# Optimization experiments

Measured on AMD Instinct MI355X. Metric: run time of the kernel, lower is better.

## Reference

```python
import jax, jax.numpy as jnp
import numpy as np

B, T, D, H, L = 8, 150, 30, 5, 3
HD = D // H  # 6
ORIG = (300, 74, 35)


def setup_inputs() -> dict:
    key = jax.random.key(0)
    ks = iter(jax.random.split(key, 40))
    def g(shape, s=0.05):
        return jax.random.normal(next(ks), shape, dtype=jnp.float32) * s
    return {
        "x_l": g((B, T, ORIG[0]), 1.0),
        "x_a": g((B, T, ORIG[1]), 1.0),
        "x_v": g((B, T, ORIG[2]), 1.0),
        "Wl": g((D, ORIG[0])),
        "Wa": g((D, ORIG[1])),
        "Wv": g((D, ORIG[2])),
        "in_w": g((2, L, 3 * D, D)),
        "in_b": jnp.zeros((2, L, 3 * D), jnp.float32),
        "out_w": g((2, L, D, D)),
        "out_b": jnp.zeros((2, L, D), jnp.float32),
        "lin1_w": g((2, L, 4 * D, D)),
        "lin1_b": jnp.zeros((2, L, 4 * D), jnp.float32),
        "lin2_w": g((2, L, D, 4 * D)),
        "lin2_b": jnp.zeros((2, L, D), jnp.float32),
        "n1_g": jnp.ones((2, L, D), jnp.float32),
        "n1_b": jnp.zeros((2, L, D), jnp.float32),
        "n2_g": jnp.ones((2, L, D), jnp.float32),
        "n2_b": jnp.zeros((2, L, D), jnp.float32),
        "p1_w": g((2 * D, 2 * D)),
        "p1_b": jnp.zeros((2 * D,), jnp.float32),
        "p2_w": g((2 * D, 2 * D)),
        "p2_b": jnp.zeros((2 * D,), jnp.float32),
        "ow": g((1, 2 * D)),
        "ob": jnp.zeros((1,), jnp.float32),
    }


def _ln(x, g, b, eps=1e-5):
    m = x.mean(-1, keepdims=True)
    v = jnp.var(x, axis=-1, keepdims=True)  # biased var, matches torch LayerNorm
    return (x - m) * jax.lax.rsqrt(v + eps) * g + b


def _heads(x):  # [Tt, B, D] -> [B*H, Tt, HD]
    Tt = x.shape[0]
    return x.reshape(Tt, B * H, HD).transpose(1, 0, 2)


def _layer(x, xk, xv, p):
    iw, ib, ow, ob, w1, b1, w2, b2, g1, bb1, g2, bb2 = p
    res = x
    xn, kn, vn = _ln(x, g1, bb1), _ln(xk, g1, bb1), _ln(xv, g1, bb1)
    q = (xn @ iw[:D].T + ib[:D]) * (HD ** -0.5)
    k = kn @ iw[D:2 * D].T + ib[D:2 * D]
    v = vn @ iw[2 * D:].T + ib[2 * D:]
    qh, kh, vh = _heads(q), _heads(k), _heads(v)
    # trilinear scores: [B*H, Tq, Tk, Tv]
    aw = jnp.einsum('iat,ibt,ict->iabc', qh, kh, vh)
    fused = aw.mean(-1) + aw.max(-1)          # fuse over value axis -> [B*H, Tq, Tk]
    fused = jax.nn.softmax(fused, axis=-1)
    attn = jnp.einsum('iab,ibt->iat', fused, qh)  # NB: original bmm uses q, not v
    attn = attn.transpose(1, 0, 2).reshape(-1, B, D)
    x = res + (attn @ ow.T + ob)
    res = x
    xn = _ln(x, g2, bb2)
    x = jax.nn.relu(xn @ w1.T + b1) @ w2.T + b2
    return res + x


def reference(x_l, x_a, x_v, Wl, Wa, Wv, in_w, in_b, out_w, out_b,
              lin1_w, lin1_b, lin2_w, lin2_b, n1_g, n1_b, n2_g, n2_b,
              p1_w, p1_b, p2_w, p2_b, ow, ob):
    pl = (x_l @ Wl.T).transpose(1, 0, 2)  # [T, B, D] (conv1d k=1, no bias)
    pa = (x_a @ Wa.T).transpose(1, 0, 2)
    pv = (x_v @ Wv.T).transpose(1, 0, 2)
    hs = []
    for s, (kk, vv) in enumerate(((pa, pv), (pv, pa))):
        h = pl
        for l in range(L):
            p = (in_w[s, l], in_b[s, l], out_w[s, l], out_b[s, l],
                 lin1_w[s, l], lin1_b[s, l], lin2_w[s, l], lin2_b[s, l],
                 n1_g[s, l], n1_b[s, l], n2_g[s, l], n2_b[s, l])
            h = _layer(h, kk, vv, p)
        hs.append(h[-1])  # last timestep [B, D]
    last_hs = jnp.concatenate(hs, axis=1)  # [B, 2D]
    proj = jax.nn.relu(last_hs @ p1_w.T + p1_b) @ p2_w.T + p2_b + last_hs
    out = proj @ ow.T + ob
    return (out, last_hs)
```

## Files before the change

### kernel.cpp

```cpp
#include <hip/hip_runtime.h>
#include <math.h>

#define BB 8
#define TT 150
#define DD 30
#define HH 5
#define HD 6
#define LL 3
#define NI 40
#define ROWF (TT*BB*DD)
#define RSTR 8
#define NR 152

typedef _Float16 half8 __attribute__((ext_vector_type(8)));
typedef float f32x16 __attribute__((ext_vector_type(16)));

__device__ __forceinline__ float wsum(float v) {
    #pragma unroll
    for (int m = 32; m > 0; m >>= 1) v += __shfl_xor(v, m, 64);
    return v;
}

__global__ __launch_bounds__(256) void proj3_kernel(
    const float* __restrict__ x_l, const float* __restrict__ x_a, const float* __restrict__ x_v,
    const float* __restrict__ Wl, const float* __restrict__ Wa, const float* __restrict__ Wv,
    float* __restrict__ pl, float* __restrict__ pa, float* __restrict__ pv) {
    int blk = blockIdx.x;
    int which = blk / 300;
    int w = threadIdx.x >> 6, lane = threadIdx.x & 63;
    int rowu = (blk % 300) * 4 + w;
    int t = rowu / BB, b = rowu % BB;
    const float* x = which == 0 ? x_l : (which == 1 ? x_a : x_v);
    const float* W = which == 0 ? Wl : (which == 1 ? Wa : Wv);
    float* out = which == 0 ? pl : (which == 1 ? pa : pv);
    int Cin = which == 0 ? 300 : (which == 1 ? 74 : 35);
    int cst = Cin | 1;
    __shared__ float WS[30 * 301];
    __shared__ float xr[4][304];
    for (int j = threadIdx.x; j < DD * Cin; j += 256)
        WS[(j / Cin) * cst + (j % Cin)] = W[j];
    const float* xp = x + ((size_t)b * TT + t) * Cin;
    for (int j = lane; j < Cin; j += 64) xr[w][j] = xp[j];
    __syncthreads();
    int d = lane >> 1, jh = lane & 1;
    int h1 = Cin >> 1;
    int j0 = jh ? h1 : 0, j1 = jh ? Cin : h1;
    const float* wr = WS + (size_t)(d < DD ? d : 0) * cst;
    float acc = 0.f;
    for (int j = j0; j < j1; j++) acc += xr[w][j] * wr[j];
    acc += __shfl_xor(acc, 1, 64);
    if (jh == 0 && d < DD) out[t * (BB * DD) + b * DD + d] = acc;
}

__global__ __launch_bounds__(256) void kvq0_kernel(
    const float* __restrict__ pl, const float* __restrict__ pa, const float* __restrict__ pv,
    const float* __restrict__ in_w, const float* __restrict__ in_b,
    const float* __restrict__ n1g, const float* __restrict__ n1b,
    float* __restrict__ k_all, float* __restrict__ v_all, float* __restrict__ q) {
    int blk = blockIdx.x;
    int w = threadIdx.x >> 6, lane = threadIdx.x & 63;
    __shared__ float iwS[1800];
    __shared__ float xn[4][2][30];
    if (blk < 1800) {
        int po = blk / 300;
        int s = po / LL;
        int tb = (blk % 300) * 4 + w;
        int t = tb / BB, b = tb % BB;
        const float* xk = (s == 0) ? pa : pv;
        const float* xv = (s == 0) ? pv : pa;
        const float* iw = in_w + (size_t)po * 2700 + 900;
        const float* ib = in_b + (size_t)po * 90;
        const float* g  = n1g + (size_t)po * 30;
        const float* bb = n1b + (size_t)po * 30;
        for (int j = threadIdx.x; j < 1800; j += 256) iwS[j] = iw[j];
        const float* rows[2] = { xk + (size_t)tb * 30, xv + (size_t)tb * 30 };
        for (int r = 0; r < 2; r++) {
            float xval = (lane < 30) ? rows[r][lane] : 0.f;
            float mean = wsum(xval) * (1.f / 30.f);
            float dv = (lane < 30) ? (xval - mean) : 0.f;
            float var = wsum(dv * dv) * (1.f / 30.f);
            float inv = rsqrtf(var + 1e-5f);
            if (lane < 30) xn[w][r][lane] = dv * inv * g[lane] + bb[lane];
        }
        __syncthreads();
        if (lane < 60) {
            int which = lane / 30, dd = lane % 30;
            const float* wr = iwS + lane * 30;
            const float* xv2 = xn[w][which];
            float acc = 0.f;
            #pragma unroll 6
            for (int j = 0; j < 30; j++) acc += wr[j] * xv2[j];
            acc += ib[30 + lane];
            int i = b * HH + dd / HD, hd = dd % HD;
            float* dst = which ? v_all : k_all;
            dst[((size_t)po * NI + i) * (TT * HD) + t * HD + hd] = acc;
        }
    } else {
        int r2 = blk - 1800;
        int s = r2 / 300;
        int tb = (r2 % 300) * 4 + w;
        int t = tb / BB, b = tb % BB;
        int po = s * LL;
        const float* iw = in_w + (size_t)po * 2700;
        const float* ib = in_b + (size_t)po * 90;
        const float* g  = n1g + (size_t)po * 30;
        const float* bb = n1b + (size_t)po * 30;
        for (int j = threadIdx.x; j < 900; j += 256) iwS[j] = iw[j];
        const float* row = pl + (size_t)tb * 30;
        float xval = (lane < 30) ? row[lane] : 0.f;
        float mean = wsum(xval) * (1.f / 30.f);
        float dv = (lane < 30) ? (xval - mean) : 0.f;
        float var = wsum(dv * dv) * (1.f / 30.f);
        float inv = rsqrtf(var + 1e-5f);
        if (lane < 30) xn[w][0][lane] = dv * inv * g[lane] + bb[lane];
        __syncthreads();
        if (lane < 30) {
            const float* wr = iwS + lane * 30;
            float acc = 0.f;
            #pragma unroll 6
            for (int j = 0; j < 30; j++) acc += wr[j] * xn[w][0][j];
            acc = (acc + ib[lane]) * 0.40824829046386307f;
            int i = b * HH + lane / HD, hd = lane % HD;
            q[((size_t)s * NI + i) * (TT * HD) + t * HD + hd] = acc;
        }
    }
}

__global__ __launch_bounds__(256) void score_kernel(
    const float* __restrict__ q, const float* __restrict__ k_all,
    const float* __restrict__ v_all, int l, float* __restrict__ attn) {
    int blk = blockIdx.x;
    int s = blk / 760;
    int rem = blk % 760;
    int i = rem / 19;
    int g = rem % 19;
    int tid = threadIdx.x;
    int wv = tid >> 6, lane = tid & 63;
    int lo = lane & 31, hf = lane >> 5;
    int po = s * LL + l;

    __shared__ __align__(16) _Float16 qsh[NR * RSTR];
    __shared__ __align__(16) _Float16 ksh[NR * RSTR];
    __shared__ __align__(16) _Float16 vsh[NR * RSTR];

    const float* qg = q + (size_t)(s * NI + i) * (TT * HD);
    const float* kg = k_all + (size_t)(po * NI + i) * (TT * HD);
    const float* vg = v_all + (size_t)(po * NI + i) * (TT * HD);
    half8 z8;
    #pragma unroll
    for (int t = 0; t < 8; t++) z8[t] = (_Float16)0.f;
    for (int r = tid; r < NR; r += 256) {
        half8 qa = z8, ka = z8, va = z8;
        if (r < TT) {
            #pragma unroll
            for (int t = 0; t < 6; t++) {
                qa[t] = (_Float16)qg[r * 6 + t];
                ka[t] = (_Float16)kg[r * 6 + t];
                va[t] = (_Float16)vg[r * 6 + t];
            }
        }
        *(half8*)&qsh[r * RSTR] = qa;
        *(half8*)&ksh[r * RSTR] = ka;
        *(half8*)&vsh[r * RSTR] = va;
    }
    __syncthreads();
    if (wv == 0) {
        float v6[6] = {0.f, 0.f, 0.f, 0.f, 0.f, 0.f};
        for (int c = lane; c < TT; c += 64) {
            #pragma unroll
            for (int t = 0; t < 6; t++) v6[t] += (float)vsh[c * RSTR + t];
        }
        #pragma unroll
        for (int m = 32; m > 0; m >>= 1) {
            #pragma unroll
            for (int t = 0; t < 6; t++) v6[t] += __shfl_xor(v6[t], m, 64);
        }
        if (lane < 6) vsh[TT * RSTR + lane] = (_Float16)(v6[lane] * (1.f / TT));
    }
    __syncthreads();

    f32x16 zacc;
    #pragma unroll
    for (int j = 0; j < 16; j++) zacc[j] = 0.f;

    half8 bfrag[5], vhalf[5];
    #pragma unroll
    for (int nt = 0; nt < 5; nt++) {
        int rr = nt * 32 + lo;
        int rc = rr < 151 ? rr : 151;
        half8 kf = *(const half8*)&ksh[rc * RSTR];
        half8 vf = *(const half8*)&vsh[rc * RSTR];
        bfrag[nt] = hf ? z8 : kf;
        vhalf[nt] = hf ? z8 : vf;
    }

    for (int ap = 0; ap < 2; ap++) {
        int a = g * 8 + wv * 2 + ap;
        if (a >= TT) break;
        half8 qav = *(const half8*)&qsh[a * RSTR];
        half8 afrag[5];
        #pragma unroll
        for (int nt = 0; nt < 5; nt++) afrag[nt] = vhalf[nt] * qav;

        float fsc[5];
        #pragma unroll
        for (int nb = 0; nb < 5; nb++) {
            float rm = -INFINITY;
            #pragma unroll
            for (int ma = 0; ma < 4; ma++) {
                f32x16 acc = __builtin_amdgcn_mfma_f32_32x32x16_f16(afrag[ma], bfrag[nb], zacc, 0, 0, 0);
                float m = fmaxf(acc[0], acc[1]);
                #pragma unroll
                for (int j = 2; j < 16; j += 2) m = fmaxf(fmaxf(m, acc[j]), acc[j + 1]);
                rm = fmaxf(rm, m);
            }
            f32x16 a4 = __builtin_amdgcn_mfma_f32_32x32x16_f16(afrag[4], bfrag[nb], zacc, 0, 0, 0);
            float m4 = fmaxf(a4[0], a4[1]);
            #pragma unroll
            for (int j = 2; j < 10; j += 2) m4 = fmaxf(fmaxf(m4, a4[j]), a4[j + 1]);
            float ext = (hf == 0) ? fmaxf(a4[10], a4[11]) : -INFINITY;
            rm = fmaxf(rm, fmaxf(m4, ext));
            float om = __shfl_xor(a4[10], 32, 64);
            float mn = hf ? a4[10] : om;
            rm = fmaxf(rm, __shfl_xor(rm, 32, 64));
            int bcol = nb * 32 + lo;
            fsc[nb] = (bcol < TT) ? (mn + rm) : -INFINITY;
        }
        float m = fsc[0];
        #pragma unroll
        for (int nb = 1; nb < 5; nb++) m = fmaxf(m, fsc[nb]);
        #pragma unroll
        for (int msk = 16; msk > 0; msk >>= 1) m = fmaxf(m, __shfl_xor(m, msk, 64));
        float e[5], es = 0.f;
        #pragma unroll
        for (int nb = 0; nb < 5; nb++) { e[nb] = __expf(fsc[nb] - m); es += e[nb]; }
        #pragma unroll
        for (int msk = 16; msk > 0; msk >>= 1) es += __shfl_xor(es, msk, 64);
        float acc6[6] = {0.f, 0.f, 0.f, 0.f, 0.f, 0.f};
        #pragma unroll
        for (int nb = 0; nb < 5; nb++) {
            int bcol = nb * 32 + lo;
            int bi = (bcol < TT) ? bcol : 0;
            float wgt = e[nb];
            half8 qrow = *(const half8*)&qsh[bi * RSTR];
            #pragma unroll
            for (int t = 0; t < 6; t++) acc6[t] += wgt * (float)qrow[t];
        }
        #pragma unroll
        for (int msk = 16; msk > 0; msk >>= 1) {
            #pragma unroll
            for (int t = 0; t < 6; t++) acc6[t] += __shfl_xor(acc6[t], msk, 64);
        }
        if (lane == 0) {
            float inv = 1.f / es;
            int bo = i / HH, ho = i % HH;
            float* dst = attn + (size_t)s * ROWF + a * (BB * DD) + bo * DD + ho * HD;
            #pragma unroll
            for (int t = 0; t < 6; t++) dst[t] = acc6[t] * inv;
        }
    }
}

__global__ __launch_bounds__(256) void ffnlnq_kernel(
    const float* __restrict__ attn, const float* __restrict__ pl,
    const float* __restrict__ out_w, const float* __restrict__ out_b,
    const float* __restrict__ l1w, const float* __restrict__ l1b,
    const float* __restrict__ l2w, const float* __restrict__ l2b,
    const float* __restrict__ n2g, const float* __restrict__ n2b,
    const float* __restrict__ in_w, const float* __restrict__ in_b,
    const float* __restrict__ n1g, const float* __restrict__ n1b,
    int l, int has_next,
    float* __restrict__ h, float* __restrict__ q) {
    int blk = blockIdx.x;
    int s = blk / 300;
    int w = threadIdx.x >> 6, lane = threadIdx.x & 63;
    int tb = (blk % 300) * 4 + w;
    int t = tb / BB, b = tb % BB;
    int po = s * LL + l;
    const float* ow = out_w + (size_t)po * 900;
    const float* ob = out_b + (size_t)po * 30;
    const float* w1 = l1w + (size_t)po * 3600;
    const float* b1 = l1b + (size_t)po * 120;
    const float* w2 = l2w + (size_t)po * 3600;
    const float* b2 = l2b + (size_t)po * 30;
    const float* g2 = n2g + (size_t)po * 30;
    const float* bb2 = n2b + (size_t)po * 30;
    __shared__ float owS[900];
    __shared__ float w1T[30 * 128];
    __shared__ float w2S[30 * 121];
    __shared__ float iwqS[900];
    __shared__ float arS[4][30], xnS[4][32], hidS[4][120], xqS[4][30];
    for (int j = threadIdx.x; j < 900; j += 256) owS[j] = ow[j];
    for (int j = threadIdx.x; j < 3600; j += 256) w1T[(j % 30) * 128 + (j / 30)] = w1[j];
    for (int j = threadIdx.x; j < 3600; j += 256) w2S[(j / 120) * 121 + (j % 120)] = w2[j];
    if (has_next) {
        const float* iwq = in_w + (size_t)(po + 1) * 2700;
        for (int j = threadIdx.x; j < 900; j += 256) iwqS[j] = iwq[j];
    }
    __syncthreads();
    float* hrow = h + (size_t)s * ROWF + (size_t)tb * 30;
    const float* res = (l == 0) ? (pl + (size_t)tb * 30) : hrow;
    const float* arow = attn + (size_t)s * ROWF + (size_t)tb * 30;
    if (lane < 30) arS[w][lane] = arow[lane];
    float x1v = 0.f;
    if (lane < 30) {
        const float* wr = owS + lane * 30;
        float acc = 0.f;
        #pragma unroll 6
        for (int j = 0; j < 30; j++) acc += wr[j] * arS[w][j];
        x1v = res[lane] + acc + ob[lane];
    }
    float mean = wsum(x1v) * (1.f / 30.f);
    float dv = (lane < 30) ? (x1v - mean) : 0.f;
    float var = wsum(dv * dv) * (1.f / 30.f);
    float inv = rsqrtf(var + 1e-5f);
    if (lane < 30) xnS[w][lane] = dv * inv * g2[lane] + bb2[lane];
    for (int o = lane; o < 120; o += 64) {
        float acc = 0.f;
        #pragma unroll 6
        for (int j = 0; j < 30; j++) acc += w1T[j * 128 + o] * xnS[w][j];
        hidS[w][o] = fmaxf(acc + b1[o], 0.f);
    }
    float newh = 0.f;
    if (lane < 30) {
        const float* wr = w2S + lane * 121;
        float acc = 0.f;
        #pragma unroll 8
        for (int j = 0; j < 120; j++) acc += wr[j] * hidS[w][j];
        newh = x1v + acc + b2[lane];
        hrow[lane] = newh;
    }
    if (has_next) {
        const float* g1 = n1g + (size_t)(po + 1) * 30;
        const float* bb1 = n1b + (size_t)(po + 1) * 30;
        const float* ibq = in_b + (size_t)(po + 1) * 90;
        float mean2 = wsum(newh) * (1.f / 30.f);
        float dv2 = (lane < 30) ? (newh - mean2) : 0.f;
        float var2 = wsum(dv2 * dv2) * (1.f / 30.f);
        float inv2 = rsqrtf(var2 + 1e-5f);
        if (lane < 30) xqS[w][lane] = dv2 * inv2 * g1[lane] + bb1[lane];
        if (lane < 30) {
            const float* wr = iwqS + lane * 30;
            float acc = 0.f;
            #pragma unroll 6
            for (int j = 0; j < 30; j++) acc += wr[j] * xqS[w][j];
            acc = (acc + ibq[lane]) * 0.40824829046386307f;
            int i = b * HH + lane / HD, hd = lane % HD;
            q[((size_t)s * NI + i) * (TT * HD) + t * HD + hd] = acc;
        }
    }
}

__global__ __launch_bounds__(256) void head_kernel(
    const float* __restrict__ h,
    const float* __restrict__ p1w, const float* __restrict__ p1b,
    const float* __restrict__ p2w, const float* __restrict__ p2b,
    const float* __restrict__ ow, const float* __restrict__ ob,
    float* __restrict__ out) {
    int tid = threadIdx.x;
    __shared__ float lh[480], hid[480], pr[480];
    for (int idx = tid; idx < 480; idx += 256) {
        int b = idx / 60, j = idx % 60;
        int s = j / 30, d = j % 30;
        float vv = h[(size_t)s * ROWF + 149 * (BB * DD) + b * DD + d];
        lh[idx] = vv;
        out[8 + idx] = vv;
    }
    __syncthreads();
    for (int idx = tid; idx < 480; idx += 256) {
        int b = idx / 60, o = idx % 60;
        const float* wr = p1w + o * 60;
        float acc = p1b[o];
        for (int j = 0; j < 60; j++) acc += wr[j] * lh[b * 60 + j];
        hid[idx] = fmaxf(acc, 0.f);
    }
    __syncthreads();
    for (int idx = tid; idx < 480; idx += 256) {
        int b = idx / 60, d = idx % 60;
        const float* wr = p2w + d * 60;
        float acc = p2b[d];
        for (int j = 0; j < 60; j++) acc += wr[j] * hid[b * 60 + j];
        pr[idx] = acc + lh[idx];
    }
    __syncthreads();
    if (tid < 8) {
        float acc = ob[0];
        for (int j = 0; j < 60; j++) acc += pr[tid * 60 + j] * ow[j];
        out[tid] = acc;
    }
}

extern "C" void kernel_launch(void* const* d_in, const int* in_sizes, int n_in,
                              void* d_out, int out_size, void* d_ws, size_t ws_size,
                              hipStream_t stream) {
    const float* x_l   = (const float*)d_in[0];
    const float* x_a   = (const float*)d_in[1];
    const float* x_v   = (const float*)d_in[2];
    const float* Wl    = (const float*)d_in[3];
    const float* Wa    = (const float*)d_in[4];
    const float* Wv    = (const float*)d_in[5];
    const float* in_w  = (const float*)d_in[6];
    const float* in_b  = (const float*)d_in[7];
    const float* out_w = (const float*)d_in[8];
    const float* out_b = (const float*)d_in[9];
    const float* l1w   = (const float*)d_in[10];
    const float* l1b   = (const float*)d_in[11];
    const float* l2w   = (const float*)d_in[12];
    const float* l2b   = (const float*)d_in[13];
    const float* n1g   = (const float*)d_in[14];
    const float* n1b   = (const float*)d_in[15];
    const float* n2g   = (const float*)d_in[16];
    const float* n2b   = (const float*)d_in[17];
    const float* p1w   = (const float*)d_in[18];
    const float* p1b   = (const float*)d_in[19];
    const float* p2w   = (const float*)d_in[20];
    const float* p2b   = (const float*)d_in[21];
    const float* oww   = (const float*)d_in[22];
    const float* obb   = (const float*)d_in[23];

    float* ws = (float*)d_ws;
    float* pl    = ws;
    float* pa    = ws + 36000;
    float* pv    = ws + 72000;
    float* h     = ws + 108000;
    float* q     = ws + 180000;
    float* k_all = ws + 252000;
    float* v_all = ws + 468000;
    float* at    = ws + 684000;

    proj3_kernel<<<900, 256, 0, stream>>>(x_l, x_a, x_v, Wl, Wa, Wv, pl, pa, pv);
    kvq0_kernel<<<2400, 256, 0, stream>>>(pl, pa, pv, in_w, in_b, n1g, n1b,
                                          k_all, v_all, q);
    for (int l = 0; l < LL; l++) {
        score_kernel<<<1520, 256, 0, stream>>>(q, k_all, v_all, l, at);
        ffnlnq_kernel<<<600, 256, 0, stream>>>(at, pl, out_w, out_b, l1w, l1b, l2w, l2b,
                                               n2g, n2b, in_w, in_b, n1g, n1b,
                                               l, (l < LL - 1) ? 1 : 0, h, q);
    }
    head_kernel<<<1, 256, 0, stream>>>(h, p1w, p1b, p2w, p2b, oww, obb, (float*)d_out);
}
```

Before: 243.2 us.

## Fuse input projections into kvq0 and fold head into last FFN kernel

The separate projection kernel is removed. Each K/V block now recomputes its pa/pv rows from x_a and x_v, and each Q block computes its pl row from x_l before the layer norm and Q projection. The single-block head kernel is folded into the last-layer FFN kernel: an atomic counter picks the last finishing block to compute the head. This removes two kernel launches and the pa/pv round trip through global memory. In exchange it repeats the projection across the six parameter sets, uses much more shared memory per block, and adds a fence plus atomic in every final-layer block.

```diff
diff --git a/kernel.cpp b/kernel.cpp
--- a/kernel.cpp
+++ b/kernel.cpp
@@ -21,107 +21,118 @@
     return v;
 }
 
-__global__ __launch_bounds__(256) void proj3_kernel(
+__global__ __launch_bounds__(256) void fused_pre_kernel(
     const float* __restrict__ x_l, const float* __restrict__ x_a, const float* __restrict__ x_v,
     const float* __restrict__ Wl, const float* __restrict__ Wa, const float* __restrict__ Wv,
-    float* __restrict__ pl, float* __restrict__ pa, float* __restrict__ pv) {
-    int blk = blockIdx.x;
-    int which = blk / 300;
-    int w = threadIdx.x >> 6, lane = threadIdx.x & 63;
-    int rowu = (blk % 300) * 4 + w;
-    int t = rowu / BB, b = rowu % BB;
-    const float* x = which == 0 ? x_l : (which == 1 ? x_a : x_v);
-    const float* W = which == 0 ? Wl : (which == 1 ? Wa : Wv);
-    float* out = which == 0 ? pl : (which == 1 ? pa : pv);
-    int Cin = which == 0 ? 300 : (which == 1 ? 74 : 35);
-    int cst = Cin | 1;
-    __shared__ float WS[30 * 301];
-    __shared__ float xr[4][304];
-    for (int j = threadIdx.x; j < DD * Cin; j += 256)
-        WS[(j / Cin) * cst + (j % Cin)] = W[j];
-    const float* xp = x + ((size_t)b * TT + t) * Cin;
-    for (int j = lane; j < Cin; j += 64) xr[w][j] = xp[j];
-    __syncthreads();
-    int d = lane >> 1, jh = lane & 1;
-    int h1 = Cin >> 1;
-    int j0 = jh ? h1 : 0, j1 = jh ? Cin : h1;
-    const float* wr = WS + (size_t)(d < DD ? d : 0) * cst;
-    float acc = 0.f;
-    for (int j = j0; j < j1; j++) acc += xr[w][j] * wr[j];
-    acc += __shfl_xor(acc, 1, 64);
-    if (jh == 0 && d < DD) out[t * (BB * DD) + b * DD + d] = acc;
-}
-
-__global__ __launch_bounds__(256) void kvq0_kernel(
-    const float* __restrict__ pl, const float* __restrict__ pa, const float* __restrict__ pv,
     const float* __restrict__ in_w, const float* __restrict__ in_b,
     const float* __restrict__ n1g, const float* __restrict__ n1b,
-    float* __restrict__ k_all, float* __restrict__ v_all, float* __restrict__ q) {
+    float* __restrict__ pl, float* __restrict__ k_all, float* __restrict__ v_all,
+    float* __restrict__ q, int* __restrict__ counter) {
+    __shared__ float sm[11264];
     int blk = blockIdx.x;
-    int w = threadIdx.x >> 6, lane = threadIdx.x & 63;
-    __shared__ float iwS[1800];
-    __shared__ float xn[4][2][30];
+    int tid = threadIdx.x;
+    int w = tid >> 6, lane = tid & 63;
+    if (blk == 0 && tid == 0) *counter = 0;
+
     if (blk < 1800) {
+        float* WaS = sm;
+        float* WvS = sm + 2220;
+        float* iwS = sm + 3270;
+        float* xaR = sm + 5070;
+        float* xvR = sm + 5390;
+        float* xn  = sm + 5550;
         int po = blk / 300;
         int s = po / LL;
         int tb = (blk % 300) * 4 + w;
         int t = tb / BB, b = tb % BB;
-        const float* xk = (s == 0) ? pa : pv;
-        const float* xv = (s == 0) ? pv : pa;
+        for (int j = tid; j < 2220; j += 256) WaS[j] = Wa[j];
+        for (int j = tid; j < 1050; j += 256) WvS[j] = Wv[j];
         const float* iw = in_w + (size_t)po * 2700 + 900;
-        const float* ib = in_b + (size_t)po * 90;
+        for (int j = tid; j < 1800; j += 256) iwS[j] = iw[j];
+        const float* xa = x_a + ((size_t)b * TT + t) * 74;
+        const float* xv = x_v + ((size_t)b * TT + t) * 35;
+        for (int j = lane; j < 74; j += 64) xaR[w * 80 + j] = xa[j];
+        if (lane < 35) xvR[w * 40 + lane] = xv[lane];
+        __syncthreads();
+        float pav = 0.f, pvv = 0.f;
+        if (lane < 30) {
+            const float* wr = WaS + lane * 74;
+            #pragma unroll 2
+            for (int j = 0; j < 74; j++) pav += wr[j] * xaR[w * 80 + j];
+            const float* wr2 = WvS + lane * 35;
+            #pragma unroll 5
+            for (int j = 0; j < 35; j++) pvv += wr2[j] * xvR[w * 40 + j];
+        }
         const float* g  = n1g + (size_t)po * 30;
         const float* bb = n1b + (size_t)po * 30;
-        for (int j = threadIdx.x; j < 1800; j += 256) iwS[j] = iw[j];
-        const float* rows[2] = { xk + (size_t)tb * 30, xv + (size_t)tb * 30 };
+        const float* ib = in_b + (size_t)po * 90;
+        float r01[2];
+        r01[0] = (s == 0) ? pav : pvv;
+        r01[1] = (s == 0) ? pvv : pav;
+        #pragma unroll
         for (int r = 0; r < 2; r++) {
-            float xval = (lane < 30) ? rows[r][lane] : 0.f;
+            float xval = (lane < 30) ? r01[r] : 0.f;
             float mean = wsum(xval) * (1.f / 30.f);
             float dv = (lane < 30) ? (xval - mean) : 0.f;
             float var = wsum(dv * dv) * (1.f / 30.f);
             float inv = rsqrtf(var + 1e-5f);
-            if (lane < 30) xn[w][r][lane] = dv * inv * g[lane] + bb[lane];
-        }
-        __syncthreads();
+            if (lane < 30) xn[w * 64 + r * 32 + lane] = dv * inv * g[lane] + bb[lane];
+        }
         if (lane < 60) {
             int which = lane / 30, dd = lane % 30;
             const float* wr = iwS + lane * 30;
-            const float* xv2 = xn[w][which];
+            const float* xr = xn + w * 64 + which * 32;
             float acc = 0.f;
             #pragma unroll 6
-            for (int j = 0; j < 30; j++) acc += wr[j] * xv2[j];
+            for (int j = 0; j < 30; j++) acc += wr[j] * xr[j];
             acc += ib[30 + lane];
             int i = b * HH + dd / HD, hd = dd % HD;
             float* dst = which ? v_all : k_all;
             dst[((size_t)po * NI + i) * (TT * HD) + t * HD + hd] = acc;
         }
     } else {
+        float* WlS = sm;
+        float* iwq = sm + 9000;
+        float* xlR = sm + 9900;
+        float* plR = sm + 11116;
         int r2 = blk - 1800;
         int s = r2 / 300;
         int tb = (r2 % 300) * 4 + w;
         int t = tb / BB, b = tb % BB;
         int po = s * LL;
+        for (int j = tid; j < 9000; j += 256) WlS[j] = Wl[j];
         const float* iw = in_w + (size_t)po * 2700;
-        const float* ib = in_b + (size_t)po * 90;
-        const float* g  = n1g + (size_t)po * 30;
-        const float* bb = n1b + (size_t)po * 30;
-        for (int j = threadIdx.x; j < 900; j += 256) iwS[j] = iw[j];
-        const float* row = pl + (size_t)tb * 30;
-        float xval = (lane < 30) ? row[lane] : 0.f;
+        for (int j = tid; j < 900; j += 256) iwq[j] = iw[j];
+        const float* xl = x_l + ((size_t)b * TT + t) * 300;
+        for (int j = lane; j < 300; j += 64) xlR[w * 304 + j] = xl[j];
+        __syncthreads();
+        int d = lane >> 1, jh = lane & 1;
+        const float* wr = WlS + (size_t)(d < DD ? d : 0) * 300;
+        int j0 = jh ? 150 : 0, j1 = jh ? 300 : 150;
+        float acc = 0.f;
+        for (int j = j0; j < j1; j++) acc += xlR[w * 304 + j] * wr[j];
+        acc += __shfl_xor(acc, 1, 64);
+        if (jh == 0 && d < DD) {
+            plR[w * 32 + d] = acc;
+            pl[tb * 30 + d] = acc;
+        }
+        float xval = (lane < 30) ? plR[w * 32 + lane] : 0.f;
         float mean = wsum(xval) * (1.f / 30.f);
         float dv = (lane < 30) ? (xval - mean) : 0.f;
         float var = wsum(dv * dv) * (1.f / 30.f);
         float inv = rsqrtf(var + 1e-5f);
-        if (lane < 30) xn[w][0][lane] = dv * inv * g[lane] + bb[lane];
-        __syncthreads();
+        const float* g  = n1g + (size_t)po * 30;
+        const float* bb = n1b + (size_t)po * 30;
+        const float* ib = in_b + (size_t)po * 90;
+        if (lane < 30) xlR[w * 304 + lane] = dv * inv * g[lane] + bb[lane];
         if (lane < 30) {
-            const float* wr = iwS + lane * 30;
-            float acc = 0.f;
+            const float* wrq = iwq + lane * 30;
+            float acc2 = 0.f;
             #pragma unroll 6
-            for (int j = 0; j < 30; j++) acc += wr[j] * xn[w][0][j];
-            acc = (acc + ib[lane]) * 0.40824829046386307f;
+            for (int j = 0; j < 30; j++) acc2 += wrq[j] * xlR[w * 304 + j];
+            acc2 = (acc2 + ib[lane]) * 0.40824829046386307f;
             int i = b * HH + lane / HD, hd = lane % HD;
-            q[((size_t)s * NI + i) * (TT * HD) + t * HD + hd] = acc;
+            q[((size_t)s * NI + i) * (TT * HD) + t * HD + hd] = acc2;
         }
     }
 }
@@ -269,11 +280,16 @@
     const float* __restrict__ n2g, const float* __restrict__ n2b,
     const float* __restrict__ in_w, const float* __restrict__ in_b,
     const float* __restrict__ n1g, const float* __restrict__ n1b,
+    const float* __restrict__ p1w, const float* __restrict__ p1b,
+    const float* __restrict__ p2w, const float* __restrict__ p2b,
+    const float* __restrict__ oww, const float* __restrict__ obb,
     int l, int has_next,
-    float* __restrict__ h, float* __restrict__ q) {
+    float* __restrict__ h, float* __restrict__ q,
+    int* __restrict__ counter, float* __restrict__ out) {
     int blk = blockIdx.x;
     int s = blk / 300;
-    int w = threadIdx.x >> 6, lane = threadIdx.x & 63;
+    int tid = threadIdx.x;
+    int w = tid >> 6, lane = tid & 63;
     int tb = (blk % 300) * 4 + w;
     int t = tb / BB, b = tb % BB;
     int po = s * LL + l;
@@ -290,12 +306,14 @@
     __shared__ float w2S[30 * 121];
     __shared__ float iwqS[900];
     __shared__ float arS[4][30], xnS[4][32], hidS[4][120], xqS[4][30];
-    for (int j = threadIdx.x; j < 900; j += 256) owS[j] = ow[j];
-    for (int j = threadIdx.x; j < 3600; j += 256) w1T[(j % 30) * 128 + (j / 30)] = w1[j];
-    for (int j = threadIdx.x; j < 3600; j += 256) w2S[(j / 120) * 121 + (j % 120)] = w2[j];
+    __shared__ float headS[1440];
+    __shared__ int isLast;
+    for (int j = tid; j < 900; j += 256) owS[j] = ow[j];
+    for (int j = tid; j < 3600; j += 256) w1T[(j % 30) * 128 + (j / 30)] = w1[j];
+    for (int j = tid; j < 3600; j += 256) w2S[(j / 120) * 121 + (j % 120)] = w2[j];
     if (has_next) {
         const float* iwq = in_w + (size_t)(po + 1) * 2700;
-        for (int j = threadIdx.x; j < 900; j += 256) iwqS[j] = iwq[j];
+        for (int j = tid; j < 900; j += 256) iwqS[j] = iwq[j];
     }
     __syncthreads();
     float* hrow = h + (size_t)s * ROWF + (size_t)tb * 30;
@@ -349,44 +367,50 @@
             q[((size_t)s * NI + i) * (TT * HD) + t * HD + hd] = acc;
         }
     }
-}
-
-__global__ __launch_bounds__(256) void head_kernel(
-    const float* __restrict__ h,
-    const float* __restrict__ p1w, const float* __restrict__ p1b,
-    const float* __restrict__ p2w, const float* __restrict__ p2b,
-    const float* __restrict__ ow, const float* __restrict__ ob,
-    float* __restrict__ out) {
-    int tid = threadIdx.x;
-    __shared__ float lh[480], hid[480], pr[480];
-    for (int idx = tid; idx < 480; idx += 256) {
-        int b = idx / 60, j = idx % 60;
-        int s = j / 30, d = j % 30;
-        float vv = h[(size_t)s * ROWF + 149 * (BB * DD) + b * DD + d];
-        lh[idx] = vv;
-        out[8 + idx] = vv;
-    }
-    __syncthreads();
-    for (int idx = tid; idx < 480; idx += 256) {
-        int b = idx / 60, o = idx % 60;
-        const float* wr = p1w + o * 60;
-        float acc = p1b[o];
-        for (int j = 0; j < 60; j++) acc += wr[j] * lh[b * 60 + j];
-        hid[idx] = fmaxf(acc, 0.f);
-    }
-    __syncthreads();
-    for (int idx = tid; idx < 480; idx += 256) {
-        int b = idx / 60, d = idx % 60;
-        const float* wr = p2w + d * 60;
-        float acc = p2b[d];
-        for (int j = 0; j < 60; j++) acc += wr[j] * hid[b * 60 + j];
-        pr[idx] = acc + lh[idx];
-    }
-    __syncthreads();
-    if (tid < 8) {
-        float acc = ob[0];
-        for (int j = 0; j < 60; j++) acc += pr[tid * 60 + j] * ow[j];
-        out[tid] = acc;
+
+    if (l == 2) {
+        __threadfence();
+        __syncthreads();
+        if (tid == 0) {
+            int old = atomicAdd(counter, 1);
+            isLast = (old == 599);
+        }
+        __syncthreads();
+        if (isLast) {
+            __threadfence();
+            float* lh  = headS;
+            float* hid = headS + 480;
+            float* pr  = headS + 960;
+            for (int idx = tid; idx < 480; idx += 256) {
+                int b2i = idx / 60, j = idx % 60;
+                int s2 = j / 30, d = j % 30;
+                float vv = h[(size_t)s2 * ROWF + 149 * (BB * DD) + b2i * DD + d];
+                lh[idx] = vv;
+                out[8 + idx] = vv;
+            }
+            __syncthreads();
+            for (int idx = tid; idx < 480; idx += 256) {
+                int b2i = idx / 60, o = idx % 60;
+                const float* wr = p1w + o * 60;
+                float acc = p1b[o];
+                for (int j = 0; j < 60; j++) acc += wr[j] * lh[b2i * 60 + j];
+                hid[idx] = fmaxf(acc, 0.f);
+            }
+            __syncthreads();
+            for (int idx = tid; idx < 480; idx += 256) {
+                int b2i = idx / 60, d = idx % 60;
+                const float* wr = p2w + d * 60;
+                float acc = p2b[d];
+                for (int j = 0; j < 60; j++) acc += wr[j] * hid[b2i * 60 + j];
+                pr[idx] = acc + lh[idx];
+            }
+            __syncthreads();
+            if (tid < 8) {
+                float acc = obb[0];
+                for (int j = 0; j < 60; j++) acc += pr[tid * 60 + j] * oww[j];
+                out[tid] = acc;
+            }
+        }
     }
 }
 
@@ -420,22 +444,22 @@
 
     float* ws = (float*)d_ws;
     float* pl    = ws;
-    float* pa    = ws + 36000;
-    float* pv    = ws + 72000;
     float* h     = ws + 108000;
     float* q     = ws + 180000;
     float* k_all = ws + 252000;
     float* v_all = ws + 468000;
     float* at    = ws + 684000;
-
-    proj3_kernel<<<900, 256, 0, stream>>>(x_l, x_a, x_v, Wl, Wa, Wv, pl, pa, pv);
-    kvq0_kernel<<<2400, 256, 0, stream>>>(pl, pa, pv, in_w, in_b, n1g, n1b,
-                                          k_all, v_all, q);
+    int*   cnt   = (int*)(ws + 756000);
+
+    fused_pre_kernel<<<2400, 256, 0, stream>>>(x_l, x_a, x_v, Wl, Wa, Wv,
+                                               in_w, in_b, n1g, n1b,
+                                               pl, k_all, v_all, q, cnt);
     for (int l = 0; l < LL; l++) {
         score_kernel<<<1520, 256, 0, stream>>>(q, k_all, v_all, l, at);
         ffnlnq_kernel<<<600, 256, 0, stream>>>(at, pl, out_w, out_b, l1w, l1b, l2w, l2b,
                                                n2g, n2b, in_w, in_b, n1g, n1b,
-                                               l, (l < LL - 1) ? 1 : 0, h, q);
-    }
-    head_kernel<<<1, 256, 0, stream>>>(h, p1w, p1b, p2w, p2b, oww, obb, (float*)d_out);
+                                               p1w, p1b, p2w, p2b, oww, obb,
+                                               l, (l < LL - 1) ? 1 : 0, h, q,
+                                               cnt, (float*)d_out);
+    }
 }
```

New measurement: 300.6 us. 1.24x slower.
